# Optimization experiments

Measured on AMD Instinct MI355X. Metric: run time of the kernel, lower is better.

Reference implementation:

```python
import jax, jax.numpy as jnp
import numpy as np
from jax.scipy.linalg import solve_triangular

EPS = 1e-5
CHUNK = 64

def _rms(x, w, eps=EPS):
    return x * jax.lax.rsqrt(jnp.mean(x * x, axis=-1, keepdims=True) + eps) * w

def _l2norm(x, eps=1e-6):
    return x * jax.lax.rsqrt(jnp.sum(x * x, axis=-1, keepdims=True) + eps)

def _causal_conv(x, w):
    # x: [B,T,C], w: [C,K] depthwise causal short conv
    K = w.shape[1]
    T = x.shape[1]
    xp = jnp.pad(x, ((0, 0), (K - 1, 0), (0, 0)))
    return sum(xp[:, j:j + T, :] * w[:, j] for j in range(K))

def _chunk_gated_delta_rule(q, k, v, g, beta, chunk=CHUNK):
    # q,k: [B,H,T,Dk] (l2-normalized, q pre-scaled); v: [B,H,T,Dv]; g,beta: [B,H,T]
    Bb, H, T, Dk = k.shape
    Dv = v.shape[-1]
    N = T // chunk
    qc, kc, vc = (a.reshape(Bb, H, N, chunk, -1) for a in (q, k, v))
    gc = g.reshape(Bb, H, N, chunk)
    bc = beta.reshape(Bb, H, N, chunk)
    gcs = jnp.cumsum(gc, axis=-1)  # within-chunk cumulative log-decay
    tri = jnp.tril(jnp.ones((chunk, chunk), bool))
    tri_s = jnp.tril(jnp.ones((chunk, chunk), bool), -1)
    diff = gcs[..., :, None] - gcs[..., None, :]
    decay = jnp.where(tri, jnp.exp(jnp.where(tri, diff, 0.0)), 0.0)  # [B,H,N,C,C]
    k_beta = kc * bc[..., None]
    v_beta = vc * bc[..., None]
    A = jnp.einsum('bhnck,bhndk->bhncd', k_beta, kc) * decay
    A = jnp.where(tri_s, A, 0.0)
    eye = jnp.eye(chunk, dtype=q.dtype)
    Tmat = solve_triangular(eye + A, jnp.broadcast_to(eye, A.shape), lower=True)  # (I+A)^-1
    u = Tmat @ v_beta                               # [B,H,N,C,Dv]
    w = Tmat @ (k_beta * jnp.exp(gcs)[..., None])   # [B,H,N,C,Dk]

    def step(S, inp):
        q_i, k_i, u_i, w_i, g_i, dm_i = inp
        attn = jnp.where(tri, jnp.einsum('bhck,bhdk->bhcd', q_i, k_i) * dm_i, 0.0)
        v_new = u_i - w_i @ S
        o_i = (q_i * jnp.exp(g_i)[..., None]) @ S + attn @ v_new
        g_last = g_i[..., -1]
        k_dec = k_i * jnp.exp(g_last[..., None] - g_i)[..., None]
        S = S * jnp.exp(g_last)[..., None, None] + jnp.einsum('bhck,bhcv->bhkv', k_dec, v_new)
        return S, o_i

    xs = tuple(jnp.moveaxis(a, 2, 0) for a in (qc, kc, u, w, gcs, decay))
    S0 = jnp.zeros((Bb, H, Dk, Dv), q.dtype)
    _, outs = jax.lax.scan(step, S0, xs)  # [N,B,H,C,Dv]
    return jnp.moveaxis(outs, 0, 2).reshape(Bb, H, T, Dv)

def _layer_forward(x, mask, ln1_w, qkvz_w, ba_w, conv_w, A_log, dt_bias,
                   o_norm_w, out_w, ln2_w, gate_w, up_w, down_w):
    B, T, D = x.shape
    H = A_log.shape[0]
    kd = qkvz_w.shape[0] // 4  # key_dim == value_dim here (k_heads==v_heads, Dk==Dv)
    vd = kd
    Dk = kd // H
    Dv = vd // H
    silu = jax.nn.silu
    h = _rms(x, ln1_w)
    qkvz = h @ qkvz_w.T
    q, k, v, z = jnp.split(qkvz, [kd, 2 * kd, 2 * kd + vd], axis=-1)
    b, a = jnp.split(h @ ba_w.T, 2, axis=-1)  # [B,T,H] each
    mixed = jnp.concatenate([q, k, v], axis=-1) * mask[..., None]
    mixed = silu(_causal_conv(mixed, conv_w))
    q, k, v = jnp.split(mixed, [kd, 2 * kd], axis=-1)
    q = _l2norm(q.reshape(B, T, H, Dk))
    k = _l2norm(k.reshape(B, T, H, Dk))
    v = v.reshape(B, T, H, Dv)
    beta = jax.nn.sigmoid(b) * mask[..., None]
    g = -jnp.exp(A_log) * jax.nn.softplus(a + dt_bias) * mask[..., None]
    scale = Dk ** -0.5
    bhtd = lambda t: jnp.transpose(t, (0, 2, 1, 3))
    o = _chunk_gated_delta_rule(bhtd(q) * scale, bhtd(k), bhtd(v),
                                jnp.transpose(g, (0, 2, 1)), jnp.transpose(beta, (0, 2, 1)))
    o = jnp.transpose(o, (0, 2, 1, 3))  # [B,T,H,Dv]
    o = _rms(o, o_norm_w) * silu(z.reshape(B, T, H, Dv))  # gated RMSNorm
    x = x + o.reshape(B, T, vd) @ out_w.T
    h2 = _rms(x, ln2_w)
    mlp_out = (silu(h2 @ gate_w.T) * (h2 @ up_w.T)) @ down_w.T
    return x + mlp_out

def setup_inputs():
    key = jax.random.key(0)
    ks = jax.random.split(key, 12)
    B, T, D, H, Dk, Dv, M, K = 1, 4096, 2048, 16, 128, 128, 8192, 4
    kd, vd = H * Dk, H * Dv
    nrm = lambda i, shp, sc=0.02: jax.random.normal(ks[i], shp, jnp.float32) * sc
    return {
        'x': nrm(0, (B, T, D), 1.0),
        'mask': jnp.ones((B, T), jnp.float32),
        'ln1_w': jnp.ones((D,), jnp.float32),
        'qkvz_w': nrm(1, (2 * kd + 2 * vd, D)),
        'ba_w': nrm(2, (2 * H, D)),
        'conv_w': nrm(3, (2 * kd + vd, K), 0.3),
        'A_log': jnp.log(jax.random.uniform(ks[4], (H,), jnp.float32, 1.0, 16.0)),
        'dt_bias': nrm(5, (H,), 0.5),
        'o_norm_w': jnp.ones((Dv,), jnp.float32),
        'out_w': nrm(6, (D, vd)),
        'ln2_w': jnp.ones((D,), jnp.float32),
        'gate_w': nrm(7, (M, D)),
        'up_w': nrm(8, (M, D)),
        'down_w': nrm(9, (D, M)),
    }

def reference(x, mask, ln1_w, qkvz_w, ba_w, conv_w, A_log, dt_bias,
              o_norm_w, out_w, ln2_w, gate_w, up_w, down_w):
    return _layer_forward(x, mask, ln1_w, qkvz_w, ba_w, conv_w, A_log, dt_bias,
                          o_norm_w, out_w, ln2_w, gate_w, up_w, down_w)
```

## Files before the change

### kernel.cpp

```cpp
#include <hip/hip_runtime.h>
#include <math.h>

#define T_LEN 4096
#define DMODEL 2048
#define NH 16
#define CQKV 6144
#define CQKVZ 8192
#define SCALE 0.08838834764831845f

using bf16x8 = __attribute__((ext_vector_type(8))) short;
using f32x4  = __attribute__((ext_vector_type(4))) float;

__device__ __forceinline__ float siluf(float x) { return x / (1.0f + __expf(-x)); }

__device__ __forceinline__ unsigned short f2bf(float f) {
  unsigned int u = __float_as_uint(f);
  u = (u + 0x7FFFu + ((u >> 16) & 1u)) >> 16;
  return (unsigned short)u;
}
__device__ __forceinline__ float bf2f(unsigned short u) {
  return __uint_as_float(((unsigned int)u) << 16);
}
__device__ __forceinline__ ushort4 pack4(float a, float b, float c, float d) {
  ushort4 r; r.x = f2bf(a); r.y = f2bf(b); r.z = f2bf(c); r.w = f2bf(d); return r;
}

__device__ __forceinline__ void gl_lds16(const unsigned short* g, unsigned short* l) {
  __builtin_amdgcn_global_load_lds(
      (const __attribute__((address_space(1))) void*)g,
      (__attribute__((address_space(3))) void*)l, 16, 0, 0);
}

template<int MODE>
__global__ __launch_bounds__(256) void rmsnorm_kernel(const float* __restrict__ x,
                                                      const float* __restrict__ w,
                                                      float* __restrict__ outf,
                                                      unsigned short* __restrict__ outb) {
  const int t = blockIdx.x;
  const int tid = threadIdx.x;
  const float4* xr = (const float4*)(x + (size_t)t * DMODEL);
  float4 v0 = xr[tid];
  float4 v1 = xr[tid + 256];
  float s = v0.x*v0.x + v0.y*v0.y + v0.z*v0.z + v0.w*v0.w
          + v1.x*v1.x + v1.y*v1.y + v1.z*v1.z + v1.w*v1.w;
#pragma unroll
  for (int off = 32; off > 0; off >>= 1) s += __shfl_down(s, off);
  __shared__ float red[4];
  if ((tid & 63) == 0) red[tid >> 6] = s;
  __syncthreads();
  const float tot = red[0] + red[1] + red[2] + red[3];
  const float r = rsqrtf(tot * (1.0f / DMODEL) + 1e-5f);
  const float4* wr = (const float4*)w;
  const float4 w0 = wr[tid], w1 = wr[tid + 256];
  float4 o0, o1;
  o0.x = v0.x*r*w0.x; o0.y = v0.y*r*w0.y; o0.z = v0.z*r*w0.z; o0.w = v0.w*r*w0.w;
  o1.x = v1.x*r*w1.x; o1.y = v1.y*r*w1.y; o1.z = v1.z*r*w1.z; o1.w = v1.w*r*w1.w;
  if (MODE == 1) {
    float4* orow = (float4*)(outf + (size_t)t * DMODEL);
    orow[tid] = o0;
    orow[tid + 256] = o1;
  }
  ushort4* brow = (ushort4*)(outb + (size_t)t * DMODEL);
  brow[tid] = pack4(o0.x, o0.y, o0.z, o0.w);
  brow[tid + 256] = pack4(o1.x, o1.y, o1.z, o1.w);
}

__global__ __launch_bounds__(256) void f2b_kernel(const float* __restrict__ in,
                                                  unsigned short* __restrict__ out) {
  const size_t i = (size_t)blockIdx.x * 256 + threadIdx.x;
  const float4 a = ((const float4*)in)[2 * i];
  const float4 b = ((const float4*)in)[2 * i + 1];
  ((ushort4*)out)[2 * i] = pack4(a.x, a.y, a.z, a.w);
  ((ushort4*)out)[2 * i + 1] = pack4(b.x, b.y, b.z, b.w);
}

template<int EPI, int BM>
__global__ __launch_bounds__(512, 1) void gemm256_kernel(const unsigned short* __restrict__ A,
                                                         const unsigned short* __restrict__ B,
                                                         float* __restrict__ Cf,
                                                         unsigned short* __restrict__ Cb,
                                                         int M, int N, int K) {
  constexpr int BN = 256;
  constexpr int MI = BM / 32;
  constexpr int AW = BM / 128;
  __shared__ __align__(16) unsigned short lds[3][(BM + BN) * 32];
  const int nbm = M / BM, nbn = N / BN, nwg = nbm * nbn;
  const int nt = K >> 5;
  int bmi, bni;
  {
    const int bid = blockIdx.x;
    const int cpx = nwg >> 3;
    int sc = 1;
    while (sc * sc < cpx) sc <<= 1;
    if (sc * sc > cpx) sc >>= 1;
    const int scn = (sc > 0) ? (cpx / sc) : 0;
    if ((nwg & 7) == 0 && sc > 0 && sc * scn == cpx && (nbm % sc) == 0 && (nbn % scn) == 0) {
      const int chunk = bid & 7, widx = bid >> 3;
      const int regc = nbn / scn;
      bmi = (chunk / regc) * sc + widx / scn;
      bni = (chunk % regc) * scn + widx % scn;
    } else {
      bmi = bid / nbn; bni = bid % nbn;
    }
  }
  const int bm = bmi * BM, bn = bni * BN;
  const int tid = threadIdx.x;
  const int wv = tid >> 6, ln = tid & 63;
  const int fr = ln & 15, qq = ln >> 4;
  const int wm = wv >> 2, wn = wv & 3;
  const int ra0 = wm * (BM / 2), rb0 = wn * 64;
  const int lrow = ln >> 2;
  const int lslot = ln & 3;

  f32x4 acc[MI][4];
  const f32x4 zero = {0.f, 0.f, 0.f, 0.f};
#pragma unroll
  for (int mi = 0; mi < MI; mi++)
#pragma unroll
    for (int ni = 0; ni < 4; ni++) acc[mi][ni] = zero;

  auto stageA = [&](int buf, int t) {
    const int k0 = t << 5;
#pragma unroll
    for (int q = 0; q < AW; q++) {
      const int lr = q * 128 + wv * 16 + lrow;
      const int sl = lslot ^ ((lr >> 1) & 3);
      gl_lds16(A + (size_t)(bm + lr) * K + k0 + sl * 8,
               &lds[buf][(q * 128 + wv * 16) * 32]);
    }
  };
  auto stageB = [&](int buf, int t) {
    const int k0 = t << 5;
#pragma unroll
    for (int q = 0; q < 2; q++) {
      const int lr = q * 128 + wv * 16 + lrow;
      const int sl = lslot ^ ((lr >> 1) & 3);
      gl_lds16(B + (size_t)(bn + lr) * K + k0 + sl * 8,
               &lds[buf][BM * 32 + (q * 128 + wv * 16) * 32]);
    }
  };

  stageA(0, 0); stageB(0, 0);
  stageA(1, 1); stageB(1, 1);
  if constexpr (AW == 2) asm volatile("s_waitcnt vmcnt(4)" ::: "memory");
  else                   asm volatile("s_waitcnt vmcnt(3)" ::: "memory");
  __builtin_amdgcn_s_barrier();
  asm volatile("" ::: "memory");

  for (int t = 0; t < nt; t++) {
    const int cb = t % 3;
    const int b2 = (t + 2) % 3;
    const unsigned short* lA = &lds[cb][0];
    const unsigned short* lB = &lds[cb][BM * 32];
    bf16x8 bfr[4];
#pragma unroll
    for (int ni = 0; ni < 4; ni++) {
      const int r = rb0 + ni * 16 + fr;
      bfr[ni] = *(const bf16x8*)&lB[r * 32 + ((qq ^ ((r >> 1) & 3)) << 3)];
    }
    bf16x8 afr[MI];
#pragma unroll
    for (int mi = 0; mi < MI; mi++) {
      const int r = ra0 + mi * 16 + fr;
      afr[mi] = *(const bf16x8*)&lA[r * 32 + ((qq ^ ((r >> 1) & 3)) << 3)];
    }
    if (t + 2 < nt) { stageA(b2, t + 2); stageB(b2, t + 2); }
    __builtin_amdgcn_s_setprio(1);
#pragma unroll
    for (int mi = 0; mi < MI; mi++)
#pragma unroll
      for (int ni = 0; ni < 4; ni++)
        acc[mi][ni] = __builtin_amdgcn_mfma_f32_16x16x32_bf16(afr[mi], bfr[ni], acc[mi][ni], 0, 0, 0);
    __builtin_amdgcn_s_setprio(0);
    if (t + 1 < nt) {
      asm volatile("s_waitcnt lgkmcnt(0)" ::: "memory");
      if (t + 2 < nt) {
        if constexpr (AW == 2) asm volatile("s_waitcnt vmcnt(4)" ::: "memory");
        else                   asm volatile("s_waitcnt vmcnt(3)" ::: "memory");
      } else {
        asm volatile("s_waitcnt vmcnt(0)" ::: "memory");
      }
      __builtin_amdgcn_s_barrier();
      asm volatile("" ::: "memory");
    }
  }

  const int cm4 = qq * 4;
#pragma unroll
  for (int mi = 0; mi < MI; mi++) {
#pragma unroll
    for (int ni = 0; ni < 4; ni++) {
#pragma unroll
      for (int r = 0; r < 4; r++) {
        const int grow = bm + ra0 + mi * 16 + cm4 + r;
        const int gcol = bn + rb0 + ni * 16 + fr;
        const size_t off = (size_t)grow * N + gcol;
        const float v = acc[mi][ni][r];
        if (EPI == 0) {
          Cb[off] = f2bf(v);
        } else if (EPI == 1) {
          Cf[off] += v;
        } else {
          Cb[off] = f2bf(siluf(bf2f(Cb[off])) * v);
        }
      }
    }
  }
}

__global__ __launch_bounds__(256) void ba_gemm_kernel(const float* __restrict__ h_in,
                                                      const float* __restrict__ ba_w,
                                                      float* __restrict__ ba_out) {
  __shared__ __align__(16) float hl[2048];
  __shared__ float red[32][9];
  const int t = blockIdx.x;
  const int tid = threadIdx.x;
  const float4* hr = (const float4*)(h_in + (size_t)t * DMODEL);
  ((float4*)hl)[tid] = hr[tid];
  ((float4*)hl)[tid + 256] = hr[tid + 256];
  __syncthreads();
  const int c = tid & 31;
  const int p = tid >> 5;
  const float* wrow = ba_w + (size_t)c * DMODEL + p * 256;
  const float* hrow = hl + p * 256;
  float s = 0.f;
#pragma unroll 8
  for (int k = 0; k < 256; k++) s += hrow[k] * wrow[k];
  red[c][p] = s;
  __syncthreads();
  if (tid < 32) {
    float tot = 0.f;
#pragma unroll
    for (int q = 0; q < 8; q++) tot += red[tid][q];
    ba_out[(size_t)t * 32 + tid] = tot;
  }
}

__global__ __launch_bounds__(256) void zcopy_kernel(const unsigned short* __restrict__ qkvz,
                                                    unsigned short* __restrict__ z) {
  const int idx = blockIdx.x * 256 + threadIdx.x;
  const int t = idx >> 8;
  const int c8 = (idx & 255) * 8;
  *(uint4*)(z + (size_t)t * 2048 + c8) =
      *(const uint4*)(qkvz + (size_t)t * CQKVZ + CQKV + c8);
}

__global__ __launch_bounds__(256) void conv_silu_kernel(const unsigned short* __restrict__ qkvz,
                                                        const float* __restrict__ conv_w,
                                                        const float* __restrict__ mask,
                                                        float* __restrict__ mixed) {
  const int idx = blockIdx.x * 256 + threadIdx.x;
  const int c4 = (idx % 1536) * 4;
  const int t = idx / 1536;
  const float4 w0 = *(const float4*)(conv_w + (size_t)c4 * 4);
  const float4 w1 = *(const float4*)(conv_w + (size_t)c4 * 4 + 4);
  const float4 w2 = *(const float4*)(conv_w + (size_t)c4 * 4 + 8);
  const float4 w3 = *(const float4*)(conv_w + (size_t)c4 * 4 + 12);
  const float wj0[4] = {w0.x, w0.y, w0.z, w0.w};
  const float wj1[4] = {w1.x, w1.y, w1.z, w1.w};
  const float wj2[4] = {w2.x, w2.y, w2.z, w2.w};
  const float wj3[4] = {w3.x, w3.y, w3.z, w3.w};
  float4 acc = make_float4(0.f, 0.f, 0.f, 0.f);
#pragma unroll
  for (int j = 0; j < 4; j++) {
    const int tt = t - 3 + j;
    if (tt < 0) continue;
    const float m = mask[tt];
    const ushort4 xb = *(const ushort4*)(qkvz + (size_t)tt * CQKVZ + c4);
    acc.x += bf2f(xb.x) * m * wj0[j];
    acc.y += bf2f(xb.y) * m * wj1[j];
    acc.z += bf2f(xb.z) * m * wj2[j];
    acc.w += bf2f(xb.w) * m * wj3[j];
  }
  acc.x = siluf(acc.x); acc.y = siluf(acc.y); acc.z = siluf(acc.z); acc.w = siluf(acc.w);
  *(float4*)(mixed + (size_t)t * CQKV + c4) = acc;
}

__global__ __launch_bounds__(256) void l2norm_kernel(float* __restrict__ mixed) {
  const int r = blockIdx.x * 4 + (threadIdx.x >> 6);
  const int lane = threadIdx.x & 63;
  const int t = r >> 5;
  const int hh = r & 31;
  float* p = mixed + (size_t)t * CQKV + hh * 128 + lane * 2;
  float2 v = *(float2*)p;
  float s = v.x * v.x + v.y * v.y;
#pragma unroll
  for (int off = 32; off > 0; off >>= 1) s += __shfl_down(s, off);
  s = __shfl(s, 0);
  const float rn = rsqrtf(s + 1e-6f);
  v.x *= rn; v.y *= rn;
  *(float2*)p = v;
}

__global__ __launch_bounds__(256) void beta_g_kernel(const float* __restrict__ ba,
                                                     const float* __restrict__ A_log,
                                                     const float* __restrict__ dt_bias,
                                                     const float* __restrict__ mask,
                                                     float* __restrict__ beta,
                                                     float* __restrict__ g) {
  const int idx = blockIdx.x * 256 + threadIdx.x;
  const int t = idx >> 4;
  const int h = idx & 15;
  const float b = ba[(size_t)t * 32 + h];
  const float a = ba[(size_t)t * 32 + 16 + h];
  const float m = mask[t];
  beta[idx] = m / (1.0f + expf(-b));
  const float xx = a + dt_bias[h];
  const float sp = (xx > 20.0f) ? xx : log1pf(expf(xx));
  g[idx] = -expf(A_log[h]) * sp * m;
}

__global__ __launch_bounds__(256) void gcs_kernel(const float* __restrict__ g,
                                                  float* __restrict__ gcsbuf,
                                                  float* __restrict__ edkbuf,
                                                  float* __restrict__ egqbuf,
                                                  float* __restrict__ adecbuf) {
  const int idx = blockIdx.x * 256 + threadIdx.x;
  if (idx >= 1024) return;
  const int h = idx >> 6;
  const int n = idx & 63;
  const int t0 = n * 64;
  float s = 0.f;
  for (int i = 0; i < 64; i++) {
    s += g[(size_t)(t0 + i) * NH + h];
    gcsbuf[(size_t)idx * 64 + i] = s;
  }
  const float glast = s;
  adecbuf[idx] = __expf(glast);
  for (int i = 0; i < 64; i++) {
    const float gi = gcsbuf[(size_t)idx * 64 + i];
    edkbuf[(size_t)idx * 64 + i] = __expf(glast - gi);
    egqbuf[(size_t)idx * 64 + i] = __expf(gi) * SCALE;
  }
}

__global__ __launch_bounds__(256) void pre_attn_kernel(const float* __restrict__ mixed,
                                                       const float* __restrict__ gcsbuf,
                                                       const float* __restrict__ betabuf,
                                                       float* __restrict__ abuf,
                                                       float* __restrict__ attnbuf) {
  __shared__ __align__(16) float kl[64][132];
  __shared__ float gcs_s[64];
  __shared__ float betal[64];
  const int blk = blockIdx.x;
  const int h = blk >> 6;
  const int n = blk & 63;
  const int t0 = n * 64;
  const int tid = threadIdx.x;
  if (tid < 64) {
    gcs_s[tid] = gcsbuf[(size_t)blk * 64 + tid];
    betal[tid] = betabuf[(size_t)(t0 + tid) * NH + h];
  }
#pragma unroll
  for (int rep = 0; rep < 8; rep++) {
    const int lin = rep * 256 + tid;
    const int i = lin >> 5;
    const int d = (lin & 31) * 4;
    const float4 kv = *(const float4*)(mixed + (size_t)(t0 + i) * CQKV + 2048 + h * 128 + d);
    *(float4*)&kl[i][d] = kv;
  }
  __syncthreads();
  const int cj = tid & 15;
  const int ri = tid >> 4;
  const int i0 = ri * 4, j0 = cj * 4;
  float accA[4][4], accQ[4][4];
#pragma unroll
  for (int a = 0; a < 4; a++)
#pragma unroll
    for (int b = 0; b < 4; b++) { accA[a][b] = 0.f; accQ[a][b] = 0.f; }
  const float* qbase = mixed + (size_t)t0 * CQKV + h * 128;
#pragma unroll 4
  for (int d = 0; d < 128; d++) {
    const float kj0 = kl[j0][d], kj1 = kl[j0 + 1][d], kj2 = kl[j0 + 2][d], kj3 = kl[j0 + 3][d];
#pragma unroll
    for (int a = 0; a < 4; a++) {
      const float ka = kl[i0 + a][d];
      const float qa = qbase[(size_t)(i0 + a) * CQKV + d];
      accA[a][0] += ka * kj0; accA[a][1] += ka * kj1; accA[a][2] += ka * kj2; accA[a][3] += ka * kj3;
      accQ[a][0] += qa * kj0; accQ[a][1] += qa * kj1; accQ[a][2] += qa * kj2; accQ[a][3] += qa * kj3;
    }
  }
#pragma unroll
  for (int a = 0; a < 4; a++) {
    const int i = i0 + a;
    const float gi = gcs_s[i];
    const float bi = betal[i];
    float4 Av, Qv;
    float dec;
    dec = __expf(fminf(gi - gcs_s[j0 + 0], 0.f));
    Av.x = (i > j0 + 0) ? accA[a][0] * bi * dec : 0.f;
    Qv.x = (i >= j0 + 0) ? accQ[a][0] * dec * SCALE : 0.f;
    dec = __expf(fminf(gi - gcs_s[j0 + 1], 0.f));
    Av.y = (i > j0 + 1) ? accA[a][1] * bi * dec : 0.f;
    Qv.y = (i >= j0 + 1) ? accQ[a][1] * dec * SCALE : 0.f;
    dec = __expf(fminf(gi - gcs_s[j0 + 2], 0.f));
    Av.z = (i > j0 + 2) ? accA[a][2] * bi * dec : 0.f;
    Qv.z = (i >= j0 + 2) ? accQ[a][2] * dec * SCALE : 0.f;
    dec = __expf(fminf(gi - gcs_s[j0 + 3], 0.f));
    Av.w = (i > j0 + 3) ? accA[a][3] * bi * dec : 0.f;
    Qv.w = (i >= j0 + 3) ? accQ[a][3] * dec * SCALE : 0.f;
    *(float4*)(abuf + (size_t)blk * 4096 + i * 64 + j0) = Av;
    *(float4*)(attnbuf + (size_t)blk * 4096 + i * 64 + j0) = Qv;
  }
}

__global__ __launch_bounds__(256) void pre_solve_kernel(const float* __restrict__ abuf,
                                                        const float* __restrict__ betabuf,
                                                        float* __restrict__ tbuf) {
  __shared__ float Al[64][65];
  __shared__ float Tl[64][65];
  const int blk = blockIdx.x;
  const int h = blk >> 6;
  const int n = blk & 63;
  const int t0 = n * 64;
  const int tid = threadIdx.x;
#pragma unroll
  for (int rep = 0; rep < 4; rep++) {
    const int lin = rep * 256 + tid;
    const int i = lin >> 4;
    const int j = (lin & 15) * 4;
    const float4 av = *(const float4*)(abuf + (size_t)blk * 4096 + i * 64 + j);
    Al[i][j] = av.x; Al[i][j + 1] = av.y; Al[i][j + 2] = av.z; Al[i][j + 3] = av.w;
  }
  __syncthreads();
  if (tid < 64) {
    const int j = tid;
    const float bj = betabuf[(size_t)(t0 + j) * NH + h];
    for (int i = 0; i < 64; i++) {
      float s = (i == j) ? 1.0f : 0.0f;
      for (int l = j; l < i; l++) s -= Al[i][l] * Tl[l][j];
      Tl[i][j] = s;
    }
    for (int i = j; i < 64; i++) Tl[i][j] *= bj;
  }
  __syncthreads();
#pragma unroll
  for (int rep = 0; rep < 4; rep++) {
    const int lin = rep * 256 + tid;
    const int i = lin >> 4;
    const int j = (lin & 15) * 4;
    float4 tv;
    tv.x = Tl[i][j]; tv.y = Tl[i][j + 1]; tv.z = Tl[i][j + 2]; tv.w = Tl[i][j + 3];
    *(float4*)(tbuf + (size_t)blk * 4096 + i * 64 + j) = tv;
  }
}

__global__ __launch_bounds__(256) void pre_uw_kernel(const float* __restrict__ mixed,
                                                     const float* __restrict__ tbuf,
                                                     const float* __restrict__ gcsbuf,
                                                     float* __restrict__ ubuf,
                                                     unsigned short* __restrict__ wbf) {
  __shared__ __align__(16) float Tl[64][68];
  __shared__ __align__(16) float xl[64][132];
  __shared__ float egcs[64];
  const int blk = blockIdx.x;
  const int h = blk >> 6;
  const int n = blk & 63;
  const int t0 = n * 64;
  const int tid = threadIdx.x;
  if (tid < 64) egcs[tid] = __expf(gcsbuf[(size_t)blk * 64 + tid]);
#pragma unroll
  for (int rep = 0; rep < 4; rep++) {
    const int lin = rep * 256 + tid;
    const int i = lin >> 4;
    const int j = (lin & 15) * 4;
    const float4 tv = *(const float4*)(tbuf + (size_t)blk * 4096 + i * 64 + j);
    *(float4*)&Tl[i][j] = tv;
  }
#pragma unroll
  for (int rep = 0; rep < 8; rep++) {
    const int lin = rep * 256 + tid;
    const int i = lin >> 5;
    const int d = (lin & 31) * 4;
    const float4 vv = *(const float4*)(mixed + (size_t)(t0 + i) * CQKV + 4096 + h * 128 + d);
    *(float4*)&xl[i][d] = vv;
  }
  __syncthreads();
  const int cgu = tid & 15;
  const int riu = tid >> 4;
  const int i0 = riu * 4;
  const int d0 = cgu * 8;
  float acc[4][8];
#pragma unroll
  for (int a = 0; a < 4; a++)
#pragma unroll
    for (int b = 0; b < 8; b++) acc[a][b] = 0.f;
#pragma unroll 2
  for (int j = 0; j < 64; j++) {
    const float tv[4] = {Tl[i0][j], Tl[i0 + 1][j], Tl[i0 + 2][j], Tl[i0 + 3][j]};
    const float4 x0 = *(const float4*)&xl[j][d0];
    const float4 x1 = *(const float4*)&xl[j][d0 + 4];
    const float xv[8] = {x0.x, x0.y, x0.z, x0.w, x1.x, x1.y, x1.z, x1.w};
#pragma unroll
    for (int a = 0; a < 4; a++)
#pragma unroll
      for (int b = 0; b < 8; b++) acc[a][b] += tv[a] * xv[b];
  }
#pragma unroll
  for (int a = 0; a < 4; a++) {
    float* up = ubuf + (size_t)(t0 + i0 + a) * 2048 + h * 128 + d0;
    *(float4*)up = make_float4(acc[a][0], acc[a][1], acc[a][2], acc[a][3]);
    *(float4*)(up + 4) = make_float4(acc[a][4], acc[a][5], acc[a][6], acc[a][7]);
  }
  __syncthreads();
#pragma unroll
  for (int rep = 0; rep < 8; rep++) {
    const int lin = rep * 256 + tid;
    const int i = lin >> 5;
    const int d = (lin & 31) * 4;
    float4 kv = *(const float4*)(mixed + (size_t)(t0 + i) * CQKV + 2048 + h * 128 + d);
    const float e = egcs[i];
    kv.x *= e; kv.y *= e; kv.z *= e; kv.w *= e;
    *(float4*)&xl[i][d] = kv;
  }
  __syncthreads();
#pragma unroll
  for (int a = 0; a < 4; a++)
#pragma unroll
    for (int b = 0; b < 8; b++) acc[a][b] = 0.f;
#pragma unroll 2
  for (int j = 0; j < 64; j++) {
    const float tv[4] = {Tl[i0][j], Tl[i0 + 1][j], Tl[i0 + 2][j], Tl[i0 + 3][j]};
    const float4 x0 = *(const float4*)&xl[j][d0];
    const float4 x1 = *(const float4*)&xl[j][d0 + 4];
    const float xv[8] = {x0.x, x0.y, x0.z, x0.w, x1.x, x1.y, x1.z, x1.w};
#pragma unroll
    for (int a = 0; a < 4; a++)
#pragma unroll
      for (int b = 0; b < 8; b++) acc[a][b] += tv[a] * xv[b];
  }
#pragma unroll
  for (int a = 0; a < 4; a++) {
    const int l = i0 + a;
    unsigned short* wp = wbf + (size_t)(t0 + l) * 2048 + h * 128 + ((cgu ^ (l & 7)) << 3);
    *(ushort4*)wp = pack4(-acc[a][0], -acc[a][1], -acc[a][2], -acc[a][3]);
    *(ushort4*)(wp + 4) = pack4(-acc[a][4], -acc[a][5], -acc[a][6], -acc[a][7]);
  }
}

__global__ __launch_bounds__(256) void ktrans_kernel(const float* __restrict__ mixed,
                                                     const float* __restrict__ edkbuf,
                                                     const float* __restrict__ egqbuf,
                                                     unsigned short* __restrict__ kdT,
                                                     unsigned short* __restrict__ qe) {
  __shared__ __align__(16) float kl[64][132];
  __shared__ float edk_s[64];
  __shared__ float egq_s[64];
  const int blk = blockIdx.x;
  const int h = blk >> 6;
  const int n = blk & 63;
  const int t0 = n * 64;
  const int tid = threadIdx.x;
  if (tid < 64) {
    edk_s[tid] = edkbuf[(size_t)blk * 64 + tid];
    egq_s[tid] = egqbuf[(size_t)blk * 64 + tid];
  }
#pragma unroll
  for (int q = 0; q < 8; q++) {
    const int idx = tid + q * 256;
    const int l = idx >> 5, c4 = (idx & 31) * 4;
    *(float4*)&kl[l][c4] = *(const float4*)(mixed + (size_t)(t0 + l) * CQKV + 2048 + h * 128 + c4);
  }
  __syncthreads();
#pragma unroll
  for (int q = 0; q < 4; q++) {
    const int idx = tid + q * 256;
    const int d = idx >> 3, lsl = idx & 7;
    const int l8 = lsl * 8;
    float v[8];
#pragma unroll
    for (int j = 0; j < 8; j++) v[j] = kl[l8 + j][d] * edk_s[l8 + j];
    unsigned short* p = kdT + (size_t)blk * 8192 + d * 64 + ((lsl ^ (d & 7)) << 3);
    *(ushort4*)p = pack4(v[0], v[1], v[2], v[3]);
    *(ushort4*)(p + 4) = pack4(v[4], v[5], v[6], v[7]);
  }
#pragma unroll
  for (int q = 0; q < 8; q++) {
    const int idx = tid + q * 256;
    const int i = idx >> 5, c4 = (idx & 31) * 4;
    const float4 v = *(const float4*)(mixed + (size_t)(t0 + i) * CQKV + h * 128 + c4);
    const float e = egq_s[i];
    *(ushort4*)(qe + (size_t)(t0 + i) * 2048 + h * 128 + c4) =
        pack4(v.x * e, v.y * e, v.z * e, v.w * e);
  }
}

__global__ __launch_bounds__(256, 1) void scan_kernel(const unsigned short* __restrict__ wbf,
                                                      const unsigned short* __restrict__ kdT,
                                                      const float* __restrict__ ubuf,
                                                      const float* __restrict__ adecbuf,
                                                      unsigned short* __restrict__ STb,
                                                      unsigned short* __restrict__ vtb,
                                                      const float* __restrict__ gw,
                                                      const float* __restrict__ uw,
                                                      const float* __restrict__ dw,
                                                      const float* __restrict__ ow,
                                                      const float* __restrict__ xin,
                                                      unsigned short* __restrict__ Wg,
                                                      unsigned short* __restrict__ Wu,
                                                      unsigned short* __restrict__ Wd,
                                                      unsigned short* __restrict__ Wo,
                                                      float* __restrict__ outc) {
  __shared__ __align__(16) unsigned short stage[2][16384];
  __shared__ __align__(16) unsigned short privAll[4][6144];
  if (blockIdx.x >= 16) {
    const int xb = blockIdx.x - 16;
    const int tid = threadIdx.x;
    if (xb < 26624) {
      const float* src; unsigned short* dst; size_t u;
      if (xb < 8192)       { src = gw; dst = Wg; u = (size_t)xb * 256 + tid; }
      else if (xb < 16384) { src = uw; dst = Wu; u = (size_t)(xb - 8192) * 256 + tid; }
      else if (xb < 24576) { src = dw; dst = Wd; u = (size_t)(xb - 16384) * 256 + tid; }
      else                 { src = ow; dst = Wo; u = (size_t)(xb - 24576) * 256 + tid; }
      const float4 a = ((const float4*)src)[2 * u];
      const float4 b = ((const float4*)src)[2 * u + 1];
      ((ushort4*)dst)[2 * u] = pack4(a.x, a.y, a.z, a.w);
      ((ushort4*)dst)[2 * u + 1] = pack4(b.x, b.y, b.z, b.w);
    } else {
      const size_t i = (size_t)(xb - 26624) * 256 + tid;
      ((float4*)outc)[2 * i] = ((const float4*)xin)[2 * i];
      ((float4*)outc)[2 * i + 1] = ((const float4*)xin)[2 * i + 1];
    }
    return;
  }
  const int h = blockIdx.x;
  const int tid = threadIdx.x;
  const int ln = tid & 63;
  const int wv = tid >> 6;
  const int fr = ln & 15;
  const int g  = ln >> 4;
  const int c0 = wv * 32;
  const int fsw = fr & 7;
  unsigned short* privA = &privAll[wv][0];
  unsigned short* privB = &privAll[wv][4096];
  const f32x4 zero = {0.f, 0.f, 0.f, 0.f};

  f32x4 acc2[8][2];
#pragma unroll
  for (int dt = 0; dt < 8; dt++)
#pragma unroll
    for (int ct = 0; ct < 2; ct++) acc2[dt][ct] = zero;

  auto stage_wk = [&](int buf, int n1) {
    const int t0n = n1 * 64;
    const size_t kbase = (size_t)(h * 64 + n1) * 8192;
#pragma unroll
    for (int q = 0; q < 4; q++) {
      const int rw = (wv * 4 + q) * 4 + (ln >> 4);
      gl_lds16(wbf + (size_t)(t0n + rw) * 2048 + h * 128 + (ln & 15) * 8,
               &stage[buf][(wv * 4 + q) * 512]);
      const int rk = (wv * 4 + q) * 8 + (ln >> 3);
      gl_lds16(kdT + kbase + rk * 64 + (ln & 7) * 8,
               &stage[buf][8192 + (wv * 4 + q) * 512]);
    }
  };

  stage_wk(0, 0);
  asm volatile("s_waitcnt vmcnt(0)" ::: "memory");
  __builtin_amdgcn_s_barrier();
  asm volatile("" ::: "memory");

  for (int n = 0; n < 64; n++) {
    const int blk = h * 64 + n;
    const int t0 = n * 64;
    const unsigned short* wl = &stage[n & 1][0];
    const unsigned short* kl = &stage[n & 1][8192];
    float ur[4][2][4];
#pragma unroll
    for (int lt = 0; lt < 4; lt++)
#pragma unroll
      for (int ct = 0; ct < 2; ct++)
#pragma unroll
        for (int r = 0; r < 4; r++)
          ur[lt][ct][r] = ubuf[(size_t)(t0 + lt * 16 + g * 4 + r) * 2048 + h * 128 + c0 + ct * 16 + fr];
    const float adec = adecbuf[blk];
    __builtin_amdgcn_sched_barrier(0);
    if (n + 1 < 64) stage_wk((n + 1) & 1, n + 1);
    __builtin_amdgcn_sched_barrier(0);
#pragma unroll
    for (int dt = 0; dt < 8; dt++)
#pragma unroll
      for (int ct = 0; ct < 2; ct++) {
        const int c = ct * 16 + fr;
        const int slot = dt * 2 + (g >> 1);
        const ushort4 pv = pack4(acc2[dt][ct][0], acc2[dt][ct][1], acc2[dt][ct][2], acc2[dt][ct][3]);
        *(ushort4*)&privA[c * 128 + ((slot ^ fsw) << 3) + (g & 1) * 4] = pv;
        *(ushort4*)(STb + (size_t)blk * 16384 + (c0 + c) * 128 + dt * 16 + g * 4) = pv;
      }
    f32x4 acc1[4][2];
#pragma unroll
    for (int lt = 0; lt < 4; lt++)
#pragma unroll
      for (int ct = 0; ct < 2; ct++) {
        f32x4 t;
        t[0] = ur[lt][ct][0]; t[1] = ur[lt][ct][1]; t[2] = ur[lt][ct][2]; t[3] = ur[lt][ct][3];
        acc1[lt][ct] = t;
      }
#pragma unroll
    for (int ks = 0; ks < 4; ks++) {
      const int kb = ks * 4 + g;
      bf16x8 bfr[2];
#pragma unroll
      for (int ct = 0; ct < 2; ct++)
        bfr[ct] = *(const bf16x8*)&privA[(ct * 16 + fr) * 128 + ((kb ^ fsw) << 3)];
#pragma unroll
      for (int lt = 0; lt < 4; lt++) {
        const bf16x8 a = *(const bf16x8*)&wl[(lt * 16 + fr) * 128 + ((kb ^ fsw) << 3)];
#pragma unroll
        for (int ct = 0; ct < 2; ct++)
          acc1[lt][ct] = __builtin_amdgcn_mfma_f32_16x16x32_bf16(a, bfr[ct], acc1[lt][ct], 0, 0, 0);
      }
    }
#pragma unroll
    for (int lt = 0; lt < 4; lt++)
#pragma unroll
      for (int ct = 0; ct < 2; ct++) {
        const int c = ct * 16 + fr;
        const int slot = lt * 2 + (g >> 1);
        const ushort4 pv = pack4(acc1[lt][ct][0], acc1[lt][ct][1], acc1[lt][ct][2], acc1[lt][ct][3]);
        *(ushort4*)&privB[c * 64 + ((slot ^ fsw) << 3) + (g & 1) * 4] = pv;
        *(ushort4*)(vtb + (size_t)blk * 8192 + (c0 + c) * 64 + lt * 16 + g * 4) = pv;
      }
#pragma unroll
    for (int dt = 0; dt < 8; dt++)
#pragma unroll
      for (int ct = 0; ct < 2; ct++) {
        acc2[dt][ct][0] *= adec; acc2[dt][ct][1] *= adec;
        acc2[dt][ct][2] *= adec; acc2[dt][ct][3] *= adec;
      }
#pragma unroll
    for (int ks = 0; ks < 2; ks++) {
      const int kb = ks * 4 + g;
      bf16x8 bfr[2];
#pragma unroll
      for (int ct = 0; ct < 2; ct++)
        bfr[ct] = *(const bf16x8*)&privB[(ct * 16 + fr) * 64 + ((kb ^ fsw) << 3)];
#pragma unroll
      for (int dt = 0; dt < 8; dt++) {
        const bf16x8 a = *(const bf16x8*)&kl[(dt * 16 + fr) * 64 + ((kb ^ fsw) << 3)];
#pragma unroll
        for (int ct = 0; ct < 2; ct++)
          acc2[dt][ct] = __builtin_amdgcn_mfma_f32_16x16x32_bf16(a, bfr[ct], acc2[dt][ct], 0, 0, 0);
      }
    }
    if (n + 1 < 64) {
      asm volatile("s_waitcnt lgkmcnt(0)" ::: "memory");
      __builtin_amdgcn_sched_barrier(0);
      asm volatile("s_waitcnt vmcnt(24)" ::: "memory");
      __builtin_amdgcn_sched_barrier(0);
      __builtin_amdgcn_s_barrier();
      __builtin_amdgcn_sched_barrier(0);
    }
  }
}

__global__ __launch_bounds__(256) void ocomp_kernel(const unsigned short* __restrict__ qe,
                                                    const unsigned short* __restrict__ STbuf,
                                                    const unsigned short* __restrict__ vtbuf,
                                                    const float* __restrict__ attnbuf,
                                                    const unsigned short* __restrict__ zb,
                                                    const float* __restrict__ onw,
                                                    unsigned short* __restrict__ ob) {
  __shared__ __align__(16) unsigned short STl[128 * 128];
  __shared__ __align__(16) unsigned short vtl[128 * 64];
  __shared__ __align__(16) unsigned short ql[64 * 128];
  __shared__ __align__(16) unsigned short al[64 * 64];
  const int blk = blockIdx.x;
  const int h = blk >> 6;
  const int n = blk & 63;
  const int t0 = n * 64;
  const int tid = threadIdx.x;
#pragma unroll
  for (int q = 0; q < 8; q++) {
    const int idx = tid + q * 256;
    const int c = idx >> 4, dg = idx & 15;
    *(uint4*)&STl[c * 128 + ((dg ^ (c & 7)) << 3)] =
        *(const uint4*)(STbuf + (size_t)blk * 16384 + c * 128 + dg * 8);
  }
#pragma unroll
  for (int q = 0; q < 4; q++) {
    const int idx = tid + q * 256;
    const int c = idx >> 3, lg = idx & 7;
    *(uint4*)&vtl[c * 64 + ((lg ^ (c & 7)) << 3)] =
        *(const uint4*)(vtbuf + (size_t)blk * 8192 + c * 64 + lg * 8);
  }
#pragma unroll
  for (int q = 0; q < 4; q++) {
    const int idx = tid + q * 256;
    const int i = idx >> 4, dg = idx & 15;
    *(uint4*)&ql[i * 128 + ((dg ^ (i & 7)) << 3)] =
        *(const uint4*)(qe + (size_t)(t0 + i) * 2048 + h * 128 + dg * 8);
  }
#pragma unroll
  for (int q = 0; q < 4; q++) {
    const int idx = tid + q * 256;
    const int i = idx >> 4, l4 = (idx & 15) * 4;
    const float4 v = *(const float4*)(attnbuf + (size_t)blk * 4096 + i * 64 + l4);
    *(ushort4*)&al[i * 64 + (((l4 >> 3) ^ (i & 7)) << 3) + (l4 & 7)] =
        pack4(v.x, v.y, v.z, v.w);
  }
  __syncthreads();
  const int ln = tid & 63;
  const int wv = tid >> 6;
  const int fr = ln & 15;
  const int g = ln >> 4;
  const int i0 = wv * 16;
  f32x4 acc[8];
  const f32x4 zero = {0.f, 0.f, 0.f, 0.f};
#pragma unroll
  for (int nt = 0; nt < 8; nt++) acc[nt] = zero;
#pragma unroll
  for (int ks = 0; ks < 4; ks++) {
    const int kb = ks * 4 + g;
    const int ar = i0 + fr;
    const bf16x8 a = *(const bf16x8*)&ql[ar * 128 + ((kb ^ (ar & 7)) << 3)];
#pragma unroll
    for (int nt = 0; nt < 8; nt++) {
      const int c = nt * 16 + fr;
      const bf16x8 b = *(const bf16x8*)&STl[c * 128 + ((kb ^ (c & 7)) << 3)];
      acc[nt] = __builtin_amdgcn_mfma_f32_16x16x32_bf16(a, b, acc[nt], 0, 0, 0);
    }
  }
#pragma unroll
  for (int ks = 0; ks < 2; ks++) {
    const int kb = ks * 4 + g;
    const int ar = i0 + fr;
    const bf16x8 a = *(const bf16x8*)&al[ar * 64 + ((kb ^ (ar & 7)) << 3)];
#pragma unroll
    for (int nt = 0; nt < 8; nt++) {
      const int c = nt * 16 + fr;
      const bf16x8 b = *(const bf16x8*)&vtl[c * 64 + ((kb ^ (c & 7)) << 3)];
      acc[nt] = __builtin_amdgcn_mfma_f32_16x16x32_bf16(a, b, acc[nt], 0, 0, 0);
    }
  }
  float s0 = 0.f, s1 = 0.f, s2 = 0.f, s3 = 0.f;
#pragma unroll
  for (int nt = 0; nt < 8; nt++) {
    s0 += acc[nt][0] * acc[nt][0];
    s1 += acc[nt][1] * acc[nt][1];
    s2 += acc[nt][2] * acc[nt][2];
    s3 += acc[nt][3] * acc[nt][3];
  }
#pragma unroll
  for (int m = 1; m < 16; m <<= 1) {
    s0 += __shfl_xor(s0, m);
    s1 += __shfl_xor(s1, m);
    s2 += __shfl_xor(s2, m);
    s3 += __shfl_xor(s3, m);
  }
  float rn[4];
  rn[0] = rsqrtf(s0 * (1.0f / 128.0f) + 1e-5f);
  rn[1] = rsqrtf(s1 * (1.0f / 128.0f) + 1e-5f);
  rn[2] = rsqrtf(s2 * (1.0f / 128.0f) + 1e-5f);
  rn[3] = rsqrtf(s3 * (1.0f / 128.0f) + 1e-5f);
#pragma unroll
  for (int nt = 0; nt < 8; nt++) {
    const int c = nt * 16 + fr;
    const float wn = onw[c];
#pragma unroll
    for (int r = 0; r < 4; r++) {
      const size_t off = (size_t)(t0 + i0 + g * 4 + r) * 2048 + h * 128 + c;
      const float zz = siluf(bf2f(zb[off]));
      ob[off] = f2bf(acc[nt][r] * rn[r] * wn * zz);
    }
  }
}

extern "C" void kernel_launch(void* const* d_in, const int* in_sizes, int n_in,
                              void* d_out, int out_size, void* d_ws, size_t ws_size,
                              hipStream_t stream) {
  (void)in_sizes; (void)n_in; (void)out_size;
  const float* x        = (const float*)d_in[0];
  const float* mask     = (const float*)d_in[1];
  const float* ln1_w    = (const float*)d_in[2];
  const float* qkvz_w   = (const float*)d_in[3];
  const float* ba_w     = (const float*)d_in[4];
  const float* conv_w   = (const float*)d_in[5];
  const float* A_log    = (const float*)d_in[6];
  const float* dt_bias  = (const float*)d_in[7];
  const float* o_norm_w = (const float*)d_in[8];
  const float* out_w    = (const float*)d_in[9];
  const float* ln2_w    = (const float*)d_in[10];
  const float* gate_w   = (const float*)d_in[11];
  const float* up_w     = (const float*)d_in[12];
  const float* down_w   = (const float*)d_in[13];
  float* out = (float*)d_out;

  const size_t NEED_BYTES = (size_t)75825152 * 4;
  if (ws_size < NEED_BYTES) return;

  float* ws = (float*)d_ws;
  float* mixed_buf = ws;
  unsigned short* Wg = (unsigned short*)ws;
  unsigned short* Wu = (unsigned short*)(ws + 8388608);
  unsigned short* Wd = (unsigned short*)(ws + 16777216);
  unsigned short* qkvz_bf = (unsigned short*)(ws + 25165824);
  float* u_buf = ws + 25165824;
  unsigned short* wbf = (unsigned short*)(ws + 33554432);
  unsigned short* kdT = (unsigned short*)(ws + 37748736);
  unsigned short* gate_bf = (unsigned short*)(ws + 25165824);
  unsigned short* z_bf = (unsigned short*)(ws + 41943040);
  float* h_buf = ws + 46137344;
  float* a_buf = ws + 46137344;
  unsigned short* vt_buf = (unsigned short*)(ws + 46137344);
  float* t_buf = ws + 50331648;
  unsigned short* qe_bf = (unsigned short*)(ws + 50331648);
  unsigned short* h_bf  = (unsigned short*)(ws + 54525952);
  unsigned short* ob    = (unsigned short*)(ws + 54525952);
  unsigned short* h2_bf = (unsigned short*)(ws + 54525952);
  float* attn_buf = ws + 58720256;
  unsigned short* Wq = (unsigned short*)(ws + 62914560);
  unsigned short* ST_buf = (unsigned short*)(ws + 62914560);
  unsigned short* Wo = (unsigned short*)(ws + 71303168);
  float* ba_buf   = ws + 73400320;
  float* beta_buf = ws + 73531392;
  float* g_buf    = ws + 73596928;
  float* gcs_buf  = ws + 73662464;
  float* edk_buf  = ws + 73728000;
  float* egq_buf  = ws + 73793536;
  float* adec_buf = ws + 73859072;

  rmsnorm_kernel<1><<<4096, 256, 0, stream>>>(x, ln1_w, h_buf, h_bf);
  f2b_kernel<<<8192, 256, 0, stream>>>(qkvz_w, Wq);
  gemm256_kernel<0, 256><<<512, 512, 0, stream>>>(h_bf, Wq, nullptr, qkvz_bf, 4096, 8192, 2048);
  ba_gemm_kernel<<<4096, 256, 0, stream>>>(h_buf, ba_w, ba_buf);
  zcopy_kernel<<<4096, 256, 0, stream>>>(qkvz_bf, z_bf);
  conv_silu_kernel<<<24576, 256, 0, stream>>>(qkvz_bf, conv_w, mask, mixed_buf);
  l2norm_kernel<<<32768, 256, 0, stream>>>(mixed_buf);
  beta_g_kernel<<<256, 256, 0, stream>>>(ba_buf, A_log, dt_bias, mask, beta_buf, g_buf);
  gcs_kernel<<<4, 256, 0, stream>>>(g_buf, gcs_buf, edk_buf, egq_buf, adec_buf);
  pre_attn_kernel<<<1024, 256, 0, stream>>>(mixed_buf, gcs_buf, beta_buf, a_buf, attn_buf);
  pre_solve_kernel<<<1024, 256, 0, stream>>>(a_buf, beta_buf, t_buf);
  pre_uw_kernel<<<1024, 256, 0, stream>>>(mixed_buf, t_buf, gcs_buf, u_buf, wbf);
  ktrans_kernel<<<1024, 256, 0, stream>>>(mixed_buf, edk_buf, egq_buf, kdT, qe_bf);
  scan_kernel<<<30736, 256, 0, stream>>>(wbf, kdT, u_buf, adec_buf, ST_buf, vt_buf,
                                         gate_w, up_w, down_w, out_w, x,
                                         Wg, Wu, Wd, Wo, out);
  ocomp_kernel<<<1024, 256, 0, stream>>>(qe_bf, ST_buf, vt_buf, attn_buf,
                                         z_bf, o_norm_w, ob);
  gemm256_kernel<1, 128><<<256, 512, 0, stream>>>(ob, Wo, out, nullptr, 4096, 2048, 2048);
  rmsnorm_kernel<2><<<4096, 256, 0, stream>>>(out, ln2_w, nullptr, h2_bf);
  gemm256_kernel<0, 256><<<512, 512, 0, stream>>>(h2_bf, Wg, nullptr, gate_bf, 4096, 8192, 2048);
  gemm256_kernel<2, 256><<<512, 512, 0, stream>>>(h2_bf, Wu, nullptr, gate_bf, 4096, 8192, 2048);
  gemm256_kernel<1, 128><<<256, 512, 0, stream>>>(gate_bf, Wd, out, nullptr, 4096, 2048, 8192);
}
```

Measured before the change: 1.509 ms.

## Split scan across 8 waves per head and prefetch next chunk's u values

```diff
diff --git a/kernel.cpp b/kernel.cpp
--- a/kernel.cpp
+++ b/kernel.cpp
@@ -585,7 +585,7 @@
   }
 }
 
-__global__ __launch_bounds__(256, 1) void scan_kernel(const unsigned short* __restrict__ wbf,
+__global__ __launch_bounds__(512, 1) void scan_kernel(const unsigned short* __restrict__ wbf,
                                                       const unsigned short* __restrict__ kdT,
                                                       const float* __restrict__ ubuf,
                                                       const float* __restrict__ adecbuf,
@@ -602,22 +602,22 @@
                                                       unsigned short* __restrict__ Wo,
                                                       float* __restrict__ outc) {
   __shared__ __align__(16) unsigned short stage[2][16384];
-  __shared__ __align__(16) unsigned short privAll[4][6144];
+  __shared__ __align__(16) unsigned short privAll[8][3072];
   if (blockIdx.x >= 16) {
     const int xb = blockIdx.x - 16;
     const int tid = threadIdx.x;
-    if (xb < 26624) {
+    if (xb < 13312) {
       const float* src; unsigned short* dst; size_t u;
-      if (xb < 8192)       { src = gw; dst = Wg; u = (size_t)xb * 256 + tid; }
-      else if (xb < 16384) { src = uw; dst = Wu; u = (size_t)(xb - 8192) * 256 + tid; }
-      else if (xb < 24576) { src = dw; dst = Wd; u = (size_t)(xb - 16384) * 256 + tid; }
-      else                 { src = ow; dst = Wo; u = (size_t)(xb - 24576) * 256 + tid; }
+      if (xb < 4096)       { src = gw; dst = Wg; u = (size_t)xb * 512 + tid; }
+      else if (xb < 8192)  { src = uw; dst = Wu; u = (size_t)(xb - 4096) * 512 + tid; }
+      else if (xb < 12288) { src = dw; dst = Wd; u = (size_t)(xb - 8192) * 512 + tid; }
+      else                 { src = ow; dst = Wo; u = (size_t)(xb - 12288) * 512 + tid; }
       const float4 a = ((const float4*)src)[2 * u];
       const float4 b = ((const float4*)src)[2 * u + 1];
       ((ushort4*)dst)[2 * u] = pack4(a.x, a.y, a.z, a.w);
       ((ushort4*)dst)[2 * u + 1] = pack4(b.x, b.y, b.z, b.w);
     } else {
-      const size_t i = (size_t)(xb - 26624) * 256 + tid;
+      const size_t i = (size_t)(xb - 13312) * 512 + tid;
       ((float4*)outc)[2 * i] = ((const float4*)xin)[2 * i];
       ((float4*)outc)[2 * i + 1] = ((const float4*)xin)[2 * i + 1];
     }
@@ -629,32 +629,36 @@
   const int wv = tid >> 6;
   const int fr = ln & 15;
   const int g  = ln >> 4;
-  const int c0 = wv * 32;
+  const int c0 = wv * 16;
   const int fsw = fr & 7;
   unsigned short* privA = &privAll[wv][0];
-  unsigned short* privB = &privAll[wv][4096];
+  unsigned short* privB = &privAll[wv][2048];
   const f32x4 zero = {0.f, 0.f, 0.f, 0.f};
 
-  f32x4 acc2[8][2];
-#pragma unroll
-  for (int dt = 0; dt < 8; dt++)
-#pragma unroll
-    for (int ct = 0; ct < 2; ct++) acc2[dt][ct] = zero;
+  f32x4 acc2[8];
+#pragma unroll
+  for (int dt = 0; dt < 8; dt++) acc2[dt] = zero;
 
   auto stage_wk = [&](int buf, int n1) {
     const int t0n = n1 * 64;
     const size_t kbase = (size_t)(h * 64 + n1) * 8192;
 #pragma unroll
-    for (int q = 0; q < 4; q++) {
-      const int rw = (wv * 4 + q) * 4 + (ln >> 4);
-      gl_lds16(wbf + (size_t)(t0n + rw) * 2048 + h * 128 + (ln & 15) * 8,
-               &stage[buf][(wv * 4 + q) * 512]);
-      const int rk = (wv * 4 + q) * 8 + (ln >> 3);
-      gl_lds16(kdT + kbase + rk * 64 + (ln & 7) * 8,
-               &stage[buf][8192 + (wv * 4 + q) * 512]);
+    for (int q = 0; q < 2; q++) {
+      const int m = wv * 2 + q;
+      gl_lds16(wbf + (size_t)(t0n + m * 4 + (ln >> 4)) * 2048 + h * 128 + (ln & 15) * 8,
+               &stage[buf][m * 512]);
+      gl_lds16(kdT + kbase + (m * 8 + (ln >> 3)) * 64 + (ln & 7) * 8,
+               &stage[buf][8192 + m * 512]);
     }
   };
 
+  float ur[4][4];
+#pragma unroll
+  for (int lt = 0; lt < 4; lt++)
+#pragma unroll
+    for (int r = 0; r < 4; r++)
+      ur[lt][r] = ubuf[(size_t)(lt * 16 + g * 4 + r) * 2048 + h * 128 + c0 + fr];
+  float ad = adecbuf[h * 64];
   stage_wk(0, 0);
   asm volatile("s_waitcnt vmcnt(0)" ::: "memory");
   __builtin_amdgcn_s_barrier();
@@ -662,91 +666,81 @@
 
   for (int n = 0; n < 64; n++) {
     const int blk = h * 64 + n;
-    const int t0 = n * 64;
     const unsigned short* wl = &stage[n & 1][0];
     const unsigned short* kl = &stage[n & 1][8192];
-    float ur[4][2][4];
-#pragma unroll
-    for (int lt = 0; lt < 4; lt++)
-#pragma unroll
-      for (int ct = 0; ct < 2; ct++)
-#pragma unroll
-        for (int r = 0; r < 4; r++)
-          ur[lt][ct][r] = ubuf[(size_t)(t0 + lt * 16 + g * 4 + r) * 2048 + h * 128 + c0 + ct * 16 + fr];
-    const float adec = adecbuf[blk];
-    __builtin_amdgcn_sched_barrier(0);
     if (n + 1 < 64) stage_wk((n + 1) & 1, n + 1);
     __builtin_amdgcn_sched_barrier(0);
-#pragma unroll
-    for (int dt = 0; dt < 8; dt++)
-#pragma unroll
-      for (int ct = 0; ct < 2; ct++) {
-        const int c = ct * 16 + fr;
-        const int slot = dt * 2 + (g >> 1);
-        const ushort4 pv = pack4(acc2[dt][ct][0], acc2[dt][ct][1], acc2[dt][ct][2], acc2[dt][ct][3]);
-        *(ushort4*)&privA[c * 128 + ((slot ^ fsw) << 3) + (g & 1) * 4] = pv;
-        *(ushort4*)(STb + (size_t)blk * 16384 + (c0 + c) * 128 + dt * 16 + g * 4) = pv;
-      }
-    f32x4 acc1[4][2];
-#pragma unroll
-    for (int lt = 0; lt < 4; lt++)
-#pragma unroll
-      for (int ct = 0; ct < 2; ct++) {
-        f32x4 t;
-        t[0] = ur[lt][ct][0]; t[1] = ur[lt][ct][1]; t[2] = ur[lt][ct][2]; t[3] = ur[lt][ct][3];
-        acc1[lt][ct] = t;
-      }
+    float urn[4][4];
+    float adn = 0.f;
+    if (n + 1 < 64) {
+      const int t1 = (n + 1) * 64;
+#pragma unroll
+      for (int lt = 0; lt < 4; lt++)
+#pragma unroll
+        for (int r = 0; r < 4; r++)
+          urn[lt][r] = ubuf[(size_t)(t1 + lt * 16 + g * 4 + r) * 2048 + h * 128 + c0 + fr];
+      adn = adecbuf[blk + 1];
+    } else {
+#pragma unroll
+      for (int lt = 0; lt < 4; lt++)
+#pragma unroll
+        for (int r = 0; r < 4; r++) urn[lt][r] = 0.f;
+    }
+    __builtin_amdgcn_sched_barrier(0);
+#pragma unroll
+    for (int dt = 0; dt < 8; dt++) {
+      const int slot = dt * 2 + (g >> 1);
+      const ushort4 pv = pack4(acc2[dt][0], acc2[dt][1], acc2[dt][2], acc2[dt][3]);
+      *(ushort4*)&privA[fr * 128 + ((slot ^ fsw) << 3) + (g & 1) * 4] = pv;
+      *(ushort4*)(STb + (size_t)blk * 16384 + (c0 + fr) * 128 + dt * 16 + g * 4) = pv;
+    }
+    f32x4 acc1[4];
+#pragma unroll
+    for (int lt = 0; lt < 4; lt++) {
+      f32x4 t;
+      t[0] = ur[lt][0]; t[1] = ur[lt][1]; t[2] = ur[lt][2]; t[3] = ur[lt][3];
+      acc1[lt] = t;
+    }
 #pragma unroll
     for (int ks = 0; ks < 4; ks++) {
       const int kb = ks * 4 + g;
-      bf16x8 bfr[2];
-#pragma unroll
-      for (int ct = 0; ct < 2; ct++)
-        bfr[ct] = *(const bf16x8*)&privA[(ct * 16 + fr) * 128 + ((kb ^ fsw) << 3)];
+      const bf16x8 b = *(const bf16x8*)&privA[fr * 128 + ((kb ^ fsw) << 3)];
 #pragma unroll
       for (int lt = 0; lt < 4; lt++) {
         const bf16x8 a = *(const bf16x8*)&wl[(lt * 16 + fr) * 128 + ((kb ^ fsw) << 3)];
-#pragma unroll
-        for (int ct = 0; ct < 2; ct++)
-          acc1[lt][ct] = __builtin_amdgcn_mfma_f32_16x16x32_bf16(a, bfr[ct], acc1[lt][ct], 0, 0, 0);
+        acc1[lt] = __builtin_amdgcn_mfma_f32_16x16x32_bf16(a, b, acc1[lt], 0, 0, 0);
       }
     }
 #pragma unroll
-    for (int lt = 0; lt < 4; lt++)
-#pragma unroll
-      for (int ct = 0; ct < 2; ct++) {
-        const int c = ct * 16 + fr;
-        const int slot = lt * 2 + (g >> 1);
-        const ushort4 pv = pack4(acc1[lt][ct][0], acc1[lt][ct][1], acc1[lt][ct][2], acc1[lt][ct][3]);
-        *(ushort4*)&privB[c * 64 + ((slot ^ fsw) << 3) + (g & 1) * 4] = pv;
-        *(ushort4*)(vtb + (size_t)blk * 8192 + (c0 + c) * 64 + lt * 16 + g * 4) = pv;
-      }
-#pragma unroll
-    for (int dt = 0; dt < 8; dt++)
-#pragma unroll
-      for (int ct = 0; ct < 2; ct++) {
-        acc2[dt][ct][0] *= adec; acc2[dt][ct][1] *= adec;
-        acc2[dt][ct][2] *= adec; acc2[dt][ct][3] *= adec;
-      }
+    for (int lt = 0; lt < 4; lt++) {
+      const int slot = lt * 2 + (g >> 1);
+      const ushort4 pv = pack4(acc1[lt][0], acc1[lt][1], acc1[lt][2], acc1[lt][3]);
+      *(ushort4*)&privB[fr * 64 + ((slot ^ fsw) << 3) + (g & 1) * 4] = pv;
+      *(ushort4*)(vtb + (size_t)blk * 8192 + (c0 + fr) * 64 + lt * 16 + g * 4) = pv;
+    }
+#pragma unroll
+    for (int dt = 0; dt < 8; dt++) {
+      acc2[dt][0] *= ad; acc2[dt][1] *= ad; acc2[dt][2] *= ad; acc2[dt][3] *= ad;
+    }
 #pragma unroll
     for (int ks = 0; ks < 2; ks++) {
       const int kb = ks * 4 + g;
-      bf16x8 bfr[2];
-#pragma unroll
-      for (int ct = 0; ct < 2; ct++)
-        bfr[ct] = *(const bf16x8*)&privB[(ct * 16 + fr) * 64 + ((kb ^ fsw) << 3)];
+      const bf16x8 b = *(const bf16x8*)&privB[fr * 64 + ((kb ^ fsw) << 3)];
 #pragma unroll
       for (int dt = 0; dt < 8; dt++) {
         const bf16x8 a = *(const bf16x8*)&kl[(dt * 16 + fr) * 64 + ((kb ^ fsw) << 3)];
-#pragma unroll
-        for (int ct = 0; ct < 2; ct++)
-          acc2[dt][ct] = __builtin_amdgcn_mfma_f32_16x16x32_bf16(a, bfr[ct], acc2[dt][ct], 0, 0, 0);
+        acc2[dt] = __builtin_amdgcn_mfma_f32_16x16x32_bf16(a, b, acc2[dt], 0, 0, 0);
       }
     }
+#pragma unroll
+    for (int lt = 0; lt < 4; lt++)
+#pragma unroll
+      for (int r = 0; r < 4; r++) ur[lt][r] = urn[lt][r];
+    ad = adn;
     if (n + 1 < 64) {
       asm volatile("s_waitcnt lgkmcnt(0)" ::: "memory");
       __builtin_amdgcn_sched_barrier(0);
-      asm volatile("s_waitcnt vmcnt(24)" ::: "memory");
+      asm volatile("s_waitcnt vmcnt(29)" ::: "memory");
       __builtin_amdgcn_sched_barrier(0);
       __builtin_amdgcn_s_barrier();
       __builtin_amdgcn_sched_barrier(0);
@@ -933,7 +927,7 @@
   pre_solve_kernel<<<1024, 256, 0, stream>>>(a_buf, beta_buf, t_buf);
   pre_uw_kernel<<<1024, 256, 0, stream>>>(mixed_buf, t_buf, gcs_buf, u_buf, wbf);
   ktrans_kernel<<<1024, 256, 0, stream>>>(mixed_buf, edk_buf, egq_buf, kdT, qe_bf);
-  scan_kernel<<<30736, 256, 0, stream>>>(wbf, kdT, u_buf, adec_buf, ST_buf, vt_buf,
+  scan_kernel<<<15376, 512, 0, stream>>>(wbf, kdT, u_buf, adec_buf, ST_buf, vt_buf,
                                          gate_w, up_w, down_w, out_w, x,
                                          Wg, Wu, Wd, Wo, out);
   ocomp_kernel<<<1024, 256, 0, stream>>>(qe_bf, ST_buf, vt_buf, attn_buf,
```

Result: faster. 1.469 ms (-2.7%).
